# Kernel tuning notes

Hardware: AMD Instinct MI355X
Metric: run time of the kernel (lower is better)

The kernel has to match this reference:

```python
import jax, jax.numpy as jnp
import numpy as np

B, S, D = 4, 2048, 1024


def setup_inputs() -> dict:
    key = jax.random.key(0)
    ks = jax.random.split(key, 9)
    scale = 1.0 / np.sqrt(D)
    q = jax.random.normal(ks[0], (B, S, D), dtype=jnp.float32)
    k = jax.random.normal(ks[1], (B, S, D), dtype=jnp.float32)
    v = jax.random.normal(ks[2], (B, S, D), dtype=jnp.float32)
    w_q = jax.random.uniform(ks[3], (D, D), jnp.float32, -scale, scale)
    b_q = jax.random.uniform(ks[4], (D,), jnp.float32, -scale, scale)
    w_k = jax.random.uniform(ks[5], (D, D), jnp.float32, -scale, scale)
    b_k = jax.random.uniform(ks[6], (D,), jnp.float32, -scale, scale)
    w_v = jax.random.uniform(ks[7], (D, D), jnp.float32, -scale, scale)
    b_v = jax.random.uniform(ks[8], (D,), jnp.float32, -scale, scale)
    # additive causal mask: 0 on/below diagonal, -1e9 above
    causal = jnp.where(jnp.tril(jnp.ones((S, S), dtype=bool)), 0.0, -1e9)
    mask = causal[None, :, :].astype(jnp.float32)  # [1, S, S]
    return {"q": q, "k": k, "v": v, "mask": mask,
            "w_q": w_q, "b_q": b_q, "w_k": w_k, "b_k": b_k,
            "w_v": w_v, "b_v": b_v}


def reference(q, k, v, mask, w_q, b_q, w_k, b_k, w_v, b_v):
    # nn.Linear: x @ W^T + b
    query = jnp.einsum('bsd,ed->bse', q, w_q) + b_q  # [B,S,D]
    key_ = jnp.einsum('bsd,ed->bse', k, w_k) + b_k
    value = jnp.einsum('bsd,ed->bse', v, w_v) + b_v
    inv_sqrt_dk = 1.0 / jnp.sqrt(jnp.asarray(D, dtype=query.dtype))
    att = jnp.einsum('bqd,bkd->bqk', query, key_) * inv_sqrt_dk  # [B,S,S]
    att = att + mask
    score = jax.nn.softmax(att, axis=-1)
    return jnp.einsum('bqk,bkd->bqd', score, value)  # [B,S,D]
```

## Files before the change

### kernel.cpp

```cpp
#include <hip/hip_runtime.h>
#include <hip/hip_bf16.h>

#define SS 2048
#define DD 1024
#define NB 4

typedef __attribute__((ext_vector_type(8))) short  bf8;
typedef __attribute__((ext_vector_type(4))) float  f32x4;

static __device__ __forceinline__ unsigned short f2bf(float f) {
    unsigned u = __float_as_uint(f);
    u += 0x7fffu + ((u >> 16) & 1u);
    return (unsigned short)(u >> 16);
}
static __device__ __forceinline__ float bf2f(unsigned short u) {
    return __uint_as_float((unsigned)u << 16);
}

static __device__ __forceinline__ void gload_lds16(const void* g, void* lds) {
    __builtin_amdgcn_global_load_lds((__attribute__((address_space(1))) void*)g,
                                     (__attribute__((address_space(3))) void*)lds,
                                     16, 0, 0);
}

__global__ __launch_bounds__(256)
void cvt3(const float* __restrict__ a, const float* __restrict__ b, const float* __restrict__ c,
          unsigned short* __restrict__ oa, unsigned short* __restrict__ ob,
          unsigned short* __restrict__ oc, int n4) {
    int i = blockIdx.x * 256 + threadIdx.x;
    if (i >= n4) return;
    const float* in = blockIdx.y == 0 ? a : blockIdx.y == 1 ? b : c;
    unsigned short* out = blockIdx.y == 0 ? oa : blockIdx.y == 1 ? ob : oc;
    float4 v = ((const float4*)in)[i];
    ushort4 o;
    o.x = f2bf(v.x); o.y = f2bf(v.y); o.z = f2bf(v.z); o.w = f2bf(v.w);
    ((ushort4*)out)[i] = o;
}

#define BM 128
#define BN 128
#define BK 64

template<int MODE>
__global__ __launch_bounds__(256, 2)
void gemm_bt(const unsigned short* __restrict__ A0p, const unsigned short* __restrict__ B0p,
             const float* __restrict__ bias0,
             const unsigned short* __restrict__ A1p, const unsigned short* __restrict__ B1p,
             const float* __restrict__ bias1,
             const unsigned short* __restrict__ A2p, const unsigned short* __restrict__ B2p,
             const float* __restrict__ bias2,
             void* __restrict__ Cout)
{
    constexpr int LDA = (MODE == 3) ? 2048 : 1024;
    constexpr int LDB = (MODE == 3) ? 2048 : 1024;
    constexpr int GX  = (MODE == 2) ? 16 : 8;
    constexpr int NWG = (MODE == 0) ? 512 : (MODE == 2) ? 256 : 192;
    constexpr int CPX = NWG >> 3;

    int bx, by;
    {
        int f  = (int)blockIdx.y * GX + (int)blockIdx.x;
        int f2 = (f & 7) * CPX + (f >> 3);
        bx = f2 % GX; by = f2 / GX;
    }
    const int bz = blockIdx.z;
    if (MODE == 2 && bx > by) return;

    const unsigned short* A;
    const unsigned short* Bm;
    const float* bias = nullptr;
    int len, qt = 0, nsp = 1;
    if (MODE == 0) {
        A    = (bz == 0 ? A0p : bz == 1 ? A1p : A2p) + (size_t)by * BM * LDA;
        Bm   = (bz == 0 ? B0p : bz == 1 ? B1p : B2p) + (size_t)bx * BN * LDB;
        bias = bz == 0 ? bias0 : bz == 1 ? bias1 : bias2;
        len  = 1024;
    } else if (MODE == 2) {
        A   = A0p + (size_t)bz * SS * DD + (size_t)by * BM * LDA;
        Bm  = B0p + (size_t)bz * SS * DD + (size_t)bx * BN * LDB;
        len = 1024;
    } else {
        int seg = 0;
        if (by < 8) { qt = by; nsp = 1; }
        else        { qt = 8 + ((by - 8) >> 1); seg = (by - 8) & 1; nsp = 2; }
        int ktot = (qt + 1) * 128, hk = ktot >> 1;
        int kst  = (nsp == 2 && seg) ? hk : 0;
        len = (nsp == 1) ? ktot : hk;
        A  = A0p + (size_t)bz * SS * SS + (size_t)qt * BM * LDA + kst;
        Bm = B0p + (size_t)bz * DD * SS + (size_t)bx * BN * LDB + kst;
    }

    __shared__ __align__(16) unsigned short As[BM * BK];
    __shared__ __align__(16) unsigned short Bs[BN * BK];

    const int t = threadIdx.x;
    const int l = t & 63;
    const int w = t >> 6;
    const int wr = w >> 1, wc = w & 1;

    const int srow0 = t >> 3;
    const int sswz  = (t & 7) ^ ((t >> 3) & 7);

    f32x4 zero = {0.f, 0.f, 0.f, 0.f};
    f32x4 acc[4][4];
    #pragma unroll
    for (int i = 0; i < 4; i++)
        #pragma unroll
        for (int j = 0; j < 4; j++) acc[i][j] = zero;

    const int ar = wr * 64 + (l & 15);
    const int br = wc * 64 + (l & 15);
    const int j0 = l >> 4;

    for (int kk = 0; kk < len; kk += BK) {
        #pragma unroll
        for (int j = 0; j < 4; ++j) {
            int r = srow0 + 32 * j;
            gload_lds16(A + (size_t)r * LDA + kk + sswz * 8,
                        (char*)As + (t + 256 * j) * 16);
            gload_lds16(Bm + (size_t)r * LDB + kk + sswz * 8,
                        (char*)Bs + (t + 256 * j) * 16);
        }
        __syncthreads();
        #pragma unroll
        for (int ks = 0; ks < 2; ++ks) {
            bf8 af[4], bfr[4];
            #pragma unroll
            for (int i = 0; i < 4; i++) {
                int r = ar + i * 16;
                af[i] = *(const bf8*)((char*)As + r * 128 + (((j0 + ks * 4) ^ (r & 7)) << 4));
            }
            #pragma unroll
            for (int j = 0; j < 4; j++) {
                int r = br + j * 16;
                bfr[j] = *(const bf8*)((char*)Bs + r * 128 + (((j0 + ks * 4) ^ (r & 7)) << 4));
            }
            #pragma unroll
            for (int i = 0; i < 4; i++)
                #pragma unroll
                for (int j = 0; j < 4; j++)
                    acc[i][j] = __builtin_amdgcn_mfma_f32_16x16x32_bf16(af[i], bfr[j], acc[i][j], 0, 0, 0);
        }
        __syncthreads();
    }

    const int mb = ((MODE == 3) ? qt : by) * BM + wr * 64;
    const int nb = bx * BN + wc * 64;

    if (MODE == 0) {
        float bv[4];
        #pragma unroll
        for (int j = 0; j < 4; j++) bv[j] = bias[nb + j * 16 + (l & 15)];
        if (bz < 2) {
            unsigned short* C = (unsigned short*)Cout + (size_t)bz * NB * SS * DD;
            #pragma unroll
            for (int i = 0; i < 4; i++) {
                int m0 = mb + i * 16 + ((l >> 4) << 2);
                #pragma unroll
                for (int j = 0; j < 4; j++) {
                    int n = nb + j * 16 + (l & 15);
                    #pragma unroll
                    for (int r = 0; r < 4; r++)
                        C[(size_t)(m0 + r) * DD + n] = f2bf(acc[i][j][r] + bv[j]);
                }
            }
        } else {
            unsigned short* C = (unsigned short*)Cout + (size_t)2 * NB * SS * DD;
            int batch = (by * BM) >> 11;
            #pragma unroll
            for (int i = 0; i < 4; i++) {
                int s = (mb - batch * SS) + i * 16 + ((l >> 4) << 2);
                #pragma unroll
                for (int j = 0; j < 4; j++) {
                    int n = nb + j * 16 + (l & 15);
                    ushort4 pk;
                    pk.x = f2bf(acc[i][j][0] + bv[j]);
                    pk.y = f2bf(acc[i][j][1] + bv[j]);
                    pk.z = f2bf(acc[i][j][2] + bv[j]);
                    pk.w = f2bf(acc[i][j][3] + bv[j]);
                    *(ushort4*)&C[(size_t)batch * DD * SS + (size_t)n * SS + s] = pk;
                }
            }
        }
    } else if (MODE == 2) {
        unsigned short* C = (unsigned short*)Cout + (size_t)bz * SS * SS;
        #pragma unroll
        for (int i = 0; i < 4; i++) {
            int m0 = mb + i * 16 + ((l >> 4) << 2);
            #pragma unroll
            for (int j = 0; j < 4; j++) {
                int n = nb + j * 16 + (l & 15);
                #pragma unroll
                for (int r = 0; r < 4; r++)
                    C[(size_t)(m0 + r) * SS + n] = f2bf(acc[i][j][r] * 0.03125f);
            }
        }
    } else {
        float* C = (float*)Cout + (size_t)bz * SS * DD;
        #pragma unroll
        for (int i = 0; i < 4; i++) {
            int m0 = mb + i * 16 + ((l >> 4) << 2);
            #pragma unroll
            for (int j = 0; j < 4; j++) {
                int n = nb + j * 16 + (l & 15);
                if (nsp == 1) {
                    #pragma unroll
                    for (int r = 0; r < 4; r++)
                        C[(size_t)(m0 + r) * DD + n] = acc[i][j][r];
                } else {
                    #pragma unroll
                    for (int r = 0; r < 4; r++)
                        atomicAdd(&C[(size_t)(m0 + r) * DD + n], acc[i][j][r]);
                }
            }
        }
    }
}

__global__ __launch_bounds__(256)
void softmax_causal(const unsigned short* __restrict__ Sb, unsigned short* __restrict__ P) {
    __shared__ float tm[4], tl[4];
    int row = blockIdx.x;
    int b = row >> 11, q = row & 2047;
    const unsigned short* s = Sb + ((size_t)b * SS + q) * SS;
    unsigned short* p = P + ((size_t)b * SS + q) * SS;
    int len  = q + 1;
    int len8 = len >> 3;
    int wlen = ((q >> 7) + 1) << 7;

    float m = -3e38f, lsum = 0.f;
    for (int i8 = threadIdx.x; i8 < len8; i8 += 256) {
        ushort4 u0 = ((const ushort4*)s)[i8 * 2];
        ushort4 u1 = ((const ushort4*)s)[i8 * 2 + 1];
        float v[8] = {bf2f(u0.x), bf2f(u0.y), bf2f(u0.z), bf2f(u0.w),
                      bf2f(u1.x), bf2f(u1.y), bf2f(u1.z), bf2f(u1.w)};
        float cm = v[0];
        #pragma unroll
        for (int e = 1; e < 8; ++e) cm = fmaxf(cm, v[e]);
        float cs = 0.f;
        #pragma unroll
        for (int e = 0; e < 8; ++e) cs += __expf(v[e] - cm);
        float nm = fmaxf(m, cm);
        lsum = lsum * __expf(m - nm) + cs * __expf(cm - nm);
        m = nm;
    }
    for (int i = (len8 << 3) + threadIdx.x; i < len; i += 256) {
        float v = bf2f(s[i]);
        float nm = fmaxf(m, v);
        lsum = lsum * __expf(m - nm) + __expf(v - nm);
        m = nm;
    }
    #pragma unroll
    for (int o = 32; o; o >>= 1) {
        float om = __shfl_xor(m, o);
        float ol = __shfl_xor(lsum, o);
        float nm = fmaxf(m, om);
        lsum = lsum * __expf(m - nm) + ol * __expf(om - nm);
        m = nm;
    }
    if ((threadIdx.x & 63) == 0) { tm[threadIdx.x >> 6] = m; tl[threadIdx.x >> 6] = lsum; }
    __syncthreads();
    {
        float gm = fmaxf(fmaxf(tm[0], tm[1]), fmaxf(tm[2], tm[3]));
        float gl = tl[0] * __expf(tm[0] - gm) + tl[1] * __expf(tm[1] - gm)
                 + tl[2] * __expf(tm[2] - gm) + tl[3] * __expf(tm[3] - gm);
        m = gm; lsum = gl;
    }
    float inv = 1.f / lsum;

    for (int i8 = threadIdx.x; i8 < (wlen >> 3); i8 += 256) {
        int i = i8 << 3;
        ushort4 u0 = ((const ushort4*)s)[i8 * 2];
        ushort4 u1 = ((const ushort4*)s)[i8 * 2 + 1];
        ushort4 o0, o1;
        o0.x = (i     < len) ? f2bf(__expf(bf2f(u0.x) - m) * inv) : (unsigned short)0;
        o0.y = (i + 1 < len) ? f2bf(__expf(bf2f(u0.y) - m) * inv) : (unsigned short)0;
        o0.z = (i + 2 < len) ? f2bf(__expf(bf2f(u0.z) - m) * inv) : (unsigned short)0;
        o0.w = (i + 3 < len) ? f2bf(__expf(bf2f(u0.w) - m) * inv) : (unsigned short)0;
        o1.x = (i + 4 < len) ? f2bf(__expf(bf2f(u1.x) - m) * inv) : (unsigned short)0;
        o1.y = (i + 5 < len) ? f2bf(__expf(bf2f(u1.y) - m) * inv) : (unsigned short)0;
        o1.z = (i + 6 < len) ? f2bf(__expf(bf2f(u1.z) - m) * inv) : (unsigned short)0;
        o1.w = (i + 7 < len) ? f2bf(__expf(bf2f(u1.w) - m) * inv) : (unsigned short)0;
        ((ushort4*)p)[i8 * 2]     = o0;
        ((ushort4*)p)[i8 * 2 + 1] = o1;
    }
}

extern "C" void kernel_launch(void* const* d_in, const int* in_sizes, int n_in,
                              void* d_out, int out_size, void* d_ws, size_t ws_size,
                              hipStream_t stream) {
    constexpr size_t NX = (size_t)NB * SS * DD;
    constexpr size_t NW = (size_t)DD * DD;

    const float* q   = (const float*)d_in[0];
    const float* k   = (const float*)d_in[1];
    const float* v   = (const float*)d_in[2];
    const float* w_q = (const float*)d_in[4];
    const float* b_q = (const float*)d_in[5];
    const float* w_k = (const float*)d_in[6];
    const float* b_k = (const float*)d_in[7];
    const float* w_v = (const float*)d_in[8];
    const float* b_v = (const float*)d_in[9];
    float* out = (float*)d_out;

    char* ws = (char*)d_ws;
    size_t off = 0;
    auto take = [&](size_t bytes) { char* p = ws + off; off += (bytes + 255) & ~(size_t)255; return p; };
    unsigned short* qb  = (unsigned short*)take(NX * 2);
    unsigned short* kb  = (unsigned short*)take(NX * 2);
    unsigned short* vb  = (unsigned short*)take(NX * 2);
    unsigned short* wqb = (unsigned short*)take(NW * 2);
    unsigned short* wkb = (unsigned short*)take(NW * 2);
    unsigned short* wvb = (unsigned short*)take(NW * 2);
    unsigned short* QKV = (unsigned short*)take(NX * 2 * 3);
    unsigned short* Sb  = (unsigned short*)take((size_t)NB * SS * SS * 2);
    unsigned short* Qp  = QKV;
    unsigned short* VpT = QKV + 2 * NX;
    unsigned short* P   = qb;

    dim3 blk(256);
    for (int b = 0; b < NB; ++b)
        hipMemsetAsync(out + ((size_t)b * SS + 1024) * DD, 0, (size_t)1024 * DD * 4, stream);
    cvt3<<<dim3(NX / 4 / 256, 3), blk, 0, stream>>>(q, k, v, qb, kb, vb, (int)(NX / 4));
    cvt3<<<dim3(NW / 4 / 256, 3), blk, 0, stream>>>(w_q, w_k, w_v, wqb, wkb, wvb, (int)(NW / 4));

    gemm_bt<0><<<dim3(8, 64, 3), blk, 0, stream>>>(
        qb, wqb, b_q, kb, wkb, b_k, vb, wvb, b_v, QKV);

    gemm_bt<2><<<dim3(16, 16, 4), blk, 0, stream>>>(
        Qp, Qp + NX, nullptr, nullptr, nullptr, nullptr, nullptr, nullptr, nullptr, Sb);

    softmax_causal<<<dim3(NB * SS), blk, 0, stream>>>(Sb, P);

    gemm_bt<3><<<dim3(8, 24, 4), blk, 0, stream>>>(
        P, VpT, nullptr, nullptr, nullptr, nullptr, nullptr, nullptr, nullptr, out);
}
```

Before: 190.5 us.

## Fuse fp32-to-bf16 activation conversion into projection GEMM and compact causal QK grid

The projection GEMM now loads fp32 activations directly into LDS (double-size A tile with a new swizzle) and converts them to bf16 when building MFMA fragments. This removes the separate conversion kernel and its round trip of the bf16 activation copies through memory. The QK^T GEMM launches only the 544 lower-triangular tiles, recovering tile coordinates with a sqrt-based inverse, instead of launching a full grid and returning early. The costs are more LDS per block (which may lower occupancy), repeated conversion work per N-tile, and a separate buffer for P.

Result: faster. 176.8 us (-7.2%).

```diff
diff --git a/kernel.cpp b/kernel.cpp
--- a/kernel.cpp
+++ b/kernel.cpp
@@ -15,6 +15,11 @@
 }
 static __device__ __forceinline__ float bf2f(unsigned short u) {
     return __uint_as_float((unsigned)u << 16);
+}
+static __device__ __forceinline__ unsigned short f2bf_hw(float f) {
+    union { __hip_bfloat16 h; unsigned short s; } u;
+    u.h = __float2bfloat16(f);
+    return u.s;
 }
 
 static __device__ __forceinline__ void gload_lds16(const void* g, void* lds) {
@@ -43,40 +48,50 @@
 
 template<int MODE>
 __global__ __launch_bounds__(256, 2)
-void gemm_bt(const unsigned short* __restrict__ A0p, const unsigned short* __restrict__ B0p,
+void gemm_bt(const void* __restrict__ A0v, const unsigned short* __restrict__ B0p,
              const float* __restrict__ bias0,
-             const unsigned short* __restrict__ A1p, const unsigned short* __restrict__ B1p,
+             const void* __restrict__ A1v, const unsigned short* __restrict__ B1p,
              const float* __restrict__ bias1,
-             const unsigned short* __restrict__ A2p, const unsigned short* __restrict__ B2p,
+             const void* __restrict__ A2v, const unsigned short* __restrict__ B2p,
              const float* __restrict__ bias2,
              void* __restrict__ Cout)
 {
     constexpr int LDA = (MODE == 3) ? 2048 : 1024;
     constexpr int LDB = (MODE == 3) ? 2048 : 1024;
-    constexpr int GX  = (MODE == 2) ? 16 : 8;
-    constexpr int NWG = (MODE == 0) ? 512 : (MODE == 2) ? 256 : 192;
-    constexpr int CPX = NWG >> 3;
-
-    int bx, by;
-    {
+
+    int bx, by, bz;
+    if (MODE == 2) {
+        int f  = (int)blockIdx.x;
+        int f2 = (f & 7) * 68 + (f >> 3);
+        bz = f2 / 136;
+        int r = f2 - bz * 136;
+        by = (int)((__fsqrt_rn(8.f * (float)r + 1.f) - 1.f) * 0.5f);
+        if (by > 15) by = 15;
+        while ((by + 1) * (by + 2) / 2 <= r) ++by;
+        while (by * (by + 1) / 2 > r) --by;
+        bx = r - by * (by + 1) / 2;
+    } else {
+        constexpr int GX  = 8;
+        constexpr int NWG = (MODE == 0) ? 512 : 192;
+        constexpr int CPX = NWG >> 3;
         int f  = (int)blockIdx.y * GX + (int)blockIdx.x;
         int f2 = (f & 7) * CPX + (f >> 3);
         bx = f2 % GX; by = f2 / GX;
-    }
-    const int bz = blockIdx.z;
-    if (MODE == 2 && bx > by) return;
-
-    const unsigned short* A;
+        bz = blockIdx.z;
+    }
+
+    const float* Af = nullptr;
+    const unsigned short* Ab = nullptr;
     const unsigned short* Bm;
     const float* bias = nullptr;
     int len, qt = 0, nsp = 1;
     if (MODE == 0) {
-        A    = (bz == 0 ? A0p : bz == 1 ? A1p : A2p) + (size_t)by * BM * LDA;
+        Af   = ((const float*)(bz == 0 ? A0v : bz == 1 ? A1v : A2v)) + (size_t)by * BM * LDA;
         Bm   = (bz == 0 ? B0p : bz == 1 ? B1p : B2p) + (size_t)bx * BN * LDB;
         bias = bz == 0 ? bias0 : bz == 1 ? bias1 : bias2;
         len  = 1024;
     } else if (MODE == 2) {
-        A   = A0p + (size_t)bz * SS * DD + (size_t)by * BM * LDA;
+        Ab  = (const unsigned short*)A0v + (size_t)bz * SS * DD + (size_t)by * BM * LDA;
         Bm  = B0p + (size_t)bz * SS * DD + (size_t)bx * BN * LDB;
         len = 1024;
     } else {
@@ -86,11 +101,12 @@
         int ktot = (qt + 1) * 128, hk = ktot >> 1;
         int kst  = (nsp == 2 && seg) ? hk : 0;
         len = (nsp == 1) ? ktot : hk;
-        A  = A0p + (size_t)bz * SS * SS + (size_t)qt * BM * LDA + kst;
+        Ab = (const unsigned short*)A0v + (size_t)bz * SS * SS + (size_t)qt * BM * LDA + kst;
         Bm = B0p + (size_t)bz * DD * SS + (size_t)bx * BN * LDB + kst;
     }
 
-    __shared__ __align__(16) unsigned short As[BM * BK];
+    constexpr int ABYTES = (MODE == 0) ? 32768 : 16384;
+    __shared__ __align__(16) char AsB[ABYTES];
     __shared__ __align__(16) unsigned short Bs[BN * BK];
 
     const int t = threadIdx.x;
@@ -113,11 +129,27 @@
     const int j0 = l >> 4;
 
     for (int kk = 0; kk < len; kk += BK) {
+        if (MODE == 0) {
+            #pragma unroll
+            for (int j = 0; j < 8; ++j) {
+                int seg = w * 8 + j;
+                int r   = seg * 4 + (l >> 4);
+                int sz  = ((r & 7) << 1) | ((r >> 3) & 1);
+                int cg  = (l & 15) ^ sz;
+                gload_lds16(Af + (size_t)r * LDA + kk + cg * 4,
+                            AsB + (size_t)(seg * 64 + l) * 16);
+            }
+        } else {
+            #pragma unroll
+            for (int j = 0; j < 4; ++j) {
+                int r = srow0 + 32 * j;
+                gload_lds16(Ab + (size_t)r * LDA + kk + sswz * 8,
+                            AsB + (t + 256 * j) * 16);
+            }
+        }
         #pragma unroll
         for (int j = 0; j < 4; ++j) {
             int r = srow0 + 32 * j;
-            gload_lds16(A + (size_t)r * LDA + kk + sswz * 8,
-                        (char*)As + (t + 256 * j) * 16);
             gload_lds16(Bm + (size_t)r * LDB + kk + sswz * 8,
                         (char*)Bs + (t + 256 * j) * 16);
         }
@@ -128,12 +160,28 @@
             #pragma unroll
             for (int i = 0; i < 4; i++) {
                 int r = ar + i * 16;
-                af[i] = *(const bf8*)((char*)As + r * 128 + (((j0 + ks * 4) ^ (r & 7)) << 4));
+                if (MODE == 0) {
+                    int sz = ((r & 7) << 1) | ((r >> 3) & 1);
+                    int c0 = ks * 8 + j0 * 2;
+                    const char* rowb = AsB + (size_t)r * 256;
+                    f32x4 lo = *(const f32x4*)(rowb + ((c0)     ^ sz) * 16);
+                    f32x4 hi = *(const f32x4*)(rowb + ((c0 + 1) ^ sz) * 16);
+                    bf8 vv;
+                    vv[0] = (short)f2bf_hw(lo[0]); vv[1] = (short)f2bf_hw(lo[1]);
+                    vv[2] = (short)f2bf_hw(lo[2]); vv[3] = (short)f2bf_hw(lo[3]);
+                    vv[4] = (short)f2bf_hw(hi[0]); vv[5] = (short)f2bf_hw(hi[1]);
+                    vv[6] = (short)f2bf_hw(hi[2]); vv[7] = (short)f2bf_hw(hi[3]);
+                    af[i] = vv;
+                } else {
+                    af[i] = *(const bf8*)(AsB + (size_t)r * 128 +
+                                          (((j0 + ks * 4) ^ (r & 7)) << 4));
+                }
             }
             #pragma unroll
             for (int j = 0; j < 4; j++) {
                 int r = br + j * 16;
-                bfr[j] = *(const bf8*)((char*)Bs + r * 128 + (((j0 + ks * 4) ^ (r & 7)) << 4));
+                bfr[j] = *(const bf8*)((char*)Bs + (size_t)r * 128 +
+                                       (((j0 + ks * 4) ^ (r & 7)) << 4));
             }
             #pragma unroll
             for (int i = 0; i < 4; i++)
@@ -306,29 +354,26 @@
     char* ws = (char*)d_ws;
     size_t off = 0;
     auto take = [&](size_t bytes) { char* p = ws + off; off += (bytes + 255) & ~(size_t)255; return p; };
-    unsigned short* qb  = (unsigned short*)take(NX * 2);
-    unsigned short* kb  = (unsigned short*)take(NX * 2);
-    unsigned short* vb  = (unsigned short*)take(NX * 2);
     unsigned short* wqb = (unsigned short*)take(NW * 2);
     unsigned short* wkb = (unsigned short*)take(NW * 2);
     unsigned short* wvb = (unsigned short*)take(NW * 2);
     unsigned short* QKV = (unsigned short*)take(NX * 2 * 3);
     unsigned short* Sb  = (unsigned short*)take((size_t)NB * SS * SS * 2);
+    unsigned short* P   = (unsigned short*)take((size_t)NB * SS * SS * 2);
     unsigned short* Qp  = QKV;
+    unsigned short* Kp  = QKV + NX;
     unsigned short* VpT = QKV + 2 * NX;
-    unsigned short* P   = qb;
 
     dim3 blk(256);
     for (int b = 0; b < NB; ++b)
         hipMemsetAsync(out + ((size_t)b * SS + 1024) * DD, 0, (size_t)1024 * DD * 4, stream);
-    cvt3<<<dim3(NX / 4 / 256, 3), blk, 0, stream>>>(q, k, v, qb, kb, vb, (int)(NX / 4));
     cvt3<<<dim3(NW / 4 / 256, 3), blk, 0, stream>>>(w_q, w_k, w_v, wqb, wkb, wvb, (int)(NW / 4));
 
     gemm_bt<0><<<dim3(8, 64, 3), blk, 0, stream>>>(
-        qb, wqb, b_q, kb, wkb, b_k, vb, wvb, b_v, QKV);
-
-    gemm_bt<2><<<dim3(16, 16, 4), blk, 0, stream>>>(
-        Qp, Qp + NX, nullptr, nullptr, nullptr, nullptr, nullptr, nullptr, nullptr, Sb);
+        q, wqb, b_q, k, wkb, b_k, v, wvb, b_v, QKV);
+
+    gemm_bt<2><<<dim3(544), blk, 0, stream>>>(
+        Qp, Kp, nullptr, nullptr, nullptr, nullptr, nullptr, nullptr, nullptr, Sb);
 
     softmax_causal<<<dim3(NB * SS), blk, 0, stream>>>(Sb, P);
 
```
